# Optimization experiments

Measured on AMD Instinct MI355X. Metric: run time of the kernel, lower is better.

Reference implementation:

```python
import jax, jax.numpy as jnp
import numpy as np

B, T, D = 2, 2048, 1024
H = 16
HD = D // H  # 64


def _rope_tables(t_len, hd, dtype=jnp.float32):
    inv_freq = 1.0 / (10000.0 ** (jnp.arange(0, hd, 2, dtype=jnp.float32) / hd))
    freqs = jnp.outer(jnp.arange(t_len, dtype=jnp.float32), inv_freq)  # [T, hd/2]
    emb = jnp.concatenate([freqs, freqs], axis=-1)  # [T, hd]
    return emb.astype(dtype)


def _rotate_half(x):
    x1, x2 = jnp.split(x, 2, axis=-1)
    return jnp.concatenate([-x2, x1], axis=-1)


def setup_inputs() -> dict:
    key = jax.random.key(0)
    k1, k2, k3 = jax.random.split(key, 3)
    x = jax.random.normal(k1, (B, T, D), dtype=jnp.float32)
    w_qkv = jax.random.normal(k2, (D, 3 * D), dtype=jnp.float32) * (D ** -0.5)
    w_out = jax.random.normal(k3, (D, D), dtype=jnp.float32) * (D ** -0.5)
    return {"x": x, "w_qkv": w_qkv, "w_out": w_out}


def reference(x, w_qkv, w_out):
    Bc, Tc, Dc = x.shape
    scale = HD ** -0.5
    qkv = x @ w_qkv  # [B,T,3D]
    q, k, v = jnp.split(qkv, 3, axis=-1)
    # -> [B,H,T,hd]
    q = q.reshape(Bc, Tc, H, HD).transpose(0, 2, 1, 3)
    k = k.reshape(Bc, Tc, H, HD).transpose(0, 2, 1, 3)
    v = v.reshape(Bc, Tc, H, HD).transpose(0, 2, 1, 3)
    emb = _rope_tables(Tc, HD, x.dtype)  # [T,hd]
    cos = jnp.cos(emb)[None, None, :, :]
    sin = jnp.sin(emb)[None, None, :, :]
    q = q * cos + _rotate_half(q) * sin
    k = k * cos + _rotate_half(k) * sin
    attn = jnp.einsum('bhqd,bhkd->bhqk', q, k) * scale  # [B,H,T,T]
    causal = jnp.tril(jnp.ones((Tc, Tc), dtype=bool))
    attn = jnp.where(causal[None, None], attn, -jnp.inf)
    attn = jax.nn.softmax(attn, axis=-1)
    out = jnp.einsum('bhqk,bhkd->bhqd', attn, v)
    out = out.transpose(0, 2, 1, 3).reshape(Bc, Tc, Dc)
    return out @ w_out
```

## Files before the change

### kernel.cpp

```cpp
#include <hip/hip_runtime.h>

#define TSEQ 2048
#define DMODEL 1024
#define NHEAD 16
#define HDIM 64
#define NB 2
#define MROWS 4096
#define NQKV 3072
#define QSCALE 0.1803368801111204f
#define NEGINF -3.0e38f

using s16x8 = __attribute__((ext_vector_type(8))) short;
using s16x4 = __attribute__((ext_vector_type(4))) short;
using f32x4 = __attribute__((ext_vector_type(4))) float;
using u32x2 = __attribute__((ext_vector_type(2))) unsigned int;

static __device__ __forceinline__ float b2f(unsigned short u) {
  union { unsigned int i; float f; } x; x.i = ((unsigned int)u) << 16; return x.f;
}
static __device__ __forceinline__ unsigned short f2b(float f) {
  unsigned int u = __float_as_uint(f);
  u += 0x7fffu + ((u >> 16) & 1u);
  return (unsigned short)(u >> 16);
}

typedef const __attribute__((address_space(1))) char gchar;
typedef __attribute__((address_space(3))) char lchar;
static __device__ __forceinline__ void gload_lds16(const void* g, void* l) {
  __builtin_amdgcn_global_load_lds((gchar*)g, (lchar*)l, 16, 0, 0);
}

__global__ __launch_bounds__(256) void k_prep(const float* __restrict__ x,
                                              short* __restrict__ xb,
                                              const float* __restrict__ wq,
                                              short* __restrict__ wqT,
                                              const float* __restrict__ wo,
                                              short* __restrict__ woT) {
  __shared__ float tile[32][33];
  const int blk = blockIdx.x;
  const int tid = threadIdx.x;
  if (blk < 4096) {
    const int i = blk * 256 + tid;
    const float4 v = ((const float4*)x)[i];
    s16x4 o;
    o.x = (short)f2b(v.x); o.y = (short)f2b(v.y);
    o.z = (short)f2b(v.z); o.w = (short)f2b(v.w);
    ((s16x4*)xb)[i] = o;
    return;
  }
  const float* in; short* out; int C, bx, by;
  if (blk < 7168) {
    const int l = blk - 4096; in = wq; out = wqT; C = NQKV;
    bx = l % 96; by = l / 96;
  } else {
    const int l = blk - 7168; in = wo; out = woT; C = DMODEL;
    bx = l & 31; by = l >> 5;
  }
  const int tx = tid & 31, ty4 = (tid >> 5) * 4;
#pragma unroll
  for (int i = 0; i < 4; ++i)
    tile[ty4 + i][tx] = in[(by * 32 + ty4 + i) * C + bx * 32 + tx];
  __syncthreads();
#pragma unroll
  for (int i = 0; i < 4; ++i)
    out[(bx * 32 + ty4 + i) * DMODEL + by * 32 + tx] = (short)f2b(tile[tx][ty4 + i]);
}

template <int IM, bool OUT_BF16>
__global__ __launch_bounds__(256) void k_gemm(const short* __restrict__ A,
                                              const short* __restrict__ BT,
                                              void* __restrict__ Cv,
                                              int M, int N, int K) {
  __shared__ __attribute__((aligned(16))) short As[IM * 32 * 32];
  __shared__ __attribute__((aligned(16))) short Bs[128 * 32];
  const int tid = threadIdx.x;
  const int wave = tid >> 6, lane = tid & 63, quad = lane >> 4, l15 = lane & 15;
  const int wm = (wave >> 1) * (IM * 16), wn = (wave & 1) * 64;
  const int m0 = blockIdx.y * (IM * 32), n0 = blockIdx.x * 128;
  f32x4 acc[IM][4] = {};
  const int r0 = tid >> 2, g0 = (tid & 3) ^ ((r0 >> 1) & 3);
  const int r1 = (tid + 256) >> 2, g1 = (tid & 3) ^ ((r1 >> 1) & 3);
  const char* Ab = (const char*)A;
  const char* Bb = (const char*)BT;
  char* AsB = (char*)As;
  char* BsB = (char*)Bs;
  const int ldsw0 = wave * 1024;
  const int ldsw1 = 4096 + wave * 1024;
  const long a0off = ((long)(m0 + r0) * K) * 2 + g0 * 16;
  const long a1off = ((long)(m0 + r1) * K) * 2 + g1 * 16;
  const long b0off = ((long)(n0 + r0) * K) * 2 + g0 * 16;
  const long b1off = ((long)(n0 + r1) * K) * 2 + g1 * 16;
  for (int k0 = 0; k0 < K; k0 += 32) {
    __syncthreads();
    gload_lds16(Ab + a0off + k0 * 2, AsB + ldsw0);
    if (IM == 4) gload_lds16(Ab + a1off + k0 * 2, AsB + ldsw1);
    gload_lds16(Bb + b0off + k0 * 2, BsB + ldsw0);
    gload_lds16(Bb + b1off + k0 * 2, BsB + ldsw1);
    __syncthreads();
    s16x8 af[IM], bf[4];
#pragma unroll
    for (int i = 0; i < IM; ++i) {
      const int ra = wm + i * 16 + l15;
      af[i] = *(const s16x8*)(AsB + ra * 64 + ((quad ^ ((ra >> 1) & 3)) * 16));
    }
#pragma unroll
    for (int j = 0; j < 4; ++j) {
      const int rb = wn + j * 16 + l15;
      bf[j] = *(const s16x8*)(BsB + rb * 64 + ((quad ^ ((rb >> 1) & 3)) * 16));
    }
#pragma unroll
    for (int i = 0; i < IM; ++i)
#pragma unroll
      for (int j = 0; j < 4; ++j)
        acc[i][j] = __builtin_amdgcn_mfma_f32_16x16x32_bf16(af[i], bf[j], acc[i][j], 0, 0, 0);
  }
#pragma unroll
  for (int i = 0; i < IM; ++i) {
    const int row = m0 + wm + i * 16 + quad * 4;
#pragma unroll
    for (int j = 0; j < 4; ++j) {
      const int col = n0 + wn + j * 16 + l15;
#pragma unroll
      for (int r = 0; r < 4; ++r) {
        if (OUT_BF16) ((short*)Cv)[(long)(row + r) * N + col] = (short)f2b(acc[i][j][r]);
        else          ((float*)Cv)[(long)(row + r) * N + col] = acc[i][j][r];
      }
    }
  }
}

__global__ __launch_bounds__(256) void k_rope_rearrange(const short* __restrict__ qkv,
                                                        short* __restrict__ Q,
                                                        short* __restrict__ Ko,
                                                        short* __restrict__ Vt) {
  __shared__ float vt[64][65];
  const int tt = blockIdx.x;
  const int h = blockIdx.y;
  const int b = blockIdx.z;
  const int bh = b * NHEAD + h;
  const int tid = threadIdx.x;
#pragma unroll
  for (int it = 0; it < 16; ++it) {
    const int idx = it * 256 + tid;
    const int tl = idx >> 6;
    const int d = idx & 63;
    const int t = tt * 64 + tl;
    const int base = (b * TSEQ + t) * NQKV + h * HDIM + d;
    const float qv = b2f((unsigned short)qkv[base]);
    const float kv = b2f((unsigned short)qkv[base + DMODEL]);
    const float vv = b2f((unsigned short)qkv[base + 2 * DMODEL]);
    const int pd = (d < 32) ? 32 : -32;
    const float qp = b2f((unsigned short)qkv[base + pd]);
    const float kp = b2f((unsigned short)qkv[base + DMODEL + pd]);
    const int fi = d & 31;
    const float inv = exp2f(-(float)fi * (13.2877123795494f / 32.0f));
    const float ang = (float)t * inv;
    float sn, cs;
    __sincosf(ang, &sn, &cs);
    const float sgn = (d < 32) ? -1.0f : 1.0f;
    const float qo = (qv * cs + sgn * qp * sn) * QSCALE;
    const float ko = kv * cs + sgn * kp * sn;
    const int ob = (bh * TSEQ + t) * HDIM + d;
    Q[ob] = (short)f2b(qo);
    Ko[ob] = (short)f2b(ko);
    vt[tl][d] = vv;
  }
  __syncthreads();
#pragma unroll
  for (int it = 0; it < 16; ++it) {
    const int idx = it * 256 + tid;
    const int d = idx >> 6;
    const int tl = idx & 63;
    Vt[(bh * HDIM + d) * TSEQ + tt * 64 + tl] = (short)f2b(vt[tl][d]);
  }
}

__global__ __launch_bounds__(256) __attribute__((amdgpu_waves_per_eu(4)))
void k_attn(const short* __restrict__ Qg,
            const short* __restrict__ Kg,
            const short* __restrict__ Vg,
            short* __restrict__ O) {
  __shared__ __attribute__((aligned(16))) short Ks[2][64 * 64];
  __shared__ __attribute__((aligned(16))) short Vs[2][64 * 64];
  __shared__ __attribute__((aligned(16))) short pl[4][16 * 64];
  const int bx = blockIdx.x, by = blockIdx.y;
  const int r_ = (bx & 7) ^ (by & 7);
  const int idx_ = ((bx >> 3) + (by >> 3)) & 3;
  const int qi = (idx_ == 0) ? r_ : (idx_ == 1) ? 15 - r_ : (idx_ == 2) ? 16 + r_ : 31 - r_;
  const int bh = by;
  const int b = bh >> 4, h = bh & 15;
  const int tid = threadIdx.x, wave = tid >> 6, lane = tid & 63;
  const int quad = lane >> 4, l15 = lane & 15;
  const char* Kb = (const char*)(Kg + (long)bh * TSEQ * HDIM);
  const char* Vb = (const char*)(Vg + (long)bh * HDIM * TSEQ);
  const short* Qb = Qg + (long)bh * TSEQ * HDIM;
  const int qr0 = qi * 64 + wave * 16;
  const s16x8 aq0 = *(const s16x8*)&Qb[(qr0 + l15) * HDIM + quad * 8];
  const s16x8 aq1 = *(const s16x8*)&Qb[(qr0 + l15) * HDIM + 32 + quad * 8];
  f32x4 o[4] = {};
  float lsum = 0.0f;
  const int kr0 = tid >> 3, kg0 = (tid & 7) ^ (kr0 & 7);
  const int kr1 = (tid + 256) >> 3, kg1 = (tid & 7) ^ (kr1 & 7);
  char* KsB = (char*)Ks;
  char* VsB = (char*)Vs;
  char* plwB = (char*)pl + wave * 2048;
  const int ldsw0 = wave * 1024, ldsw1 = 4096 + wave * 1024;

#define STAGE(kjv, buf)                                                     \
  do {                                                                      \
    const char* Kt_ = Kb + (kjv) * 8192;                                    \
    const char* Vt_ = Vb + (kjv) * 128;                                     \
    char* kd_ = KsB + (buf) * 8192;                                         \
    char* vd_ = VsB + (buf) * 8192;                                         \
    gload_lds16(Kt_ + (kr0 * 8 + kg0) * 16, kd_ + ldsw0);                   \
    gload_lds16(Kt_ + (kr1 * 8 + kg1) * 16, kd_ + ldsw1);                   \
    gload_lds16(Vt_ + kr0 * (TSEQ * 2) + kg0 * 16, vd_ + ldsw0);            \
    gload_lds16(Vt_ + kr1 * (TSEQ * 2) + kg1 * 16, vd_ + ldsw1);            \
  } while (0)

  STAGE(0, 0);
  __syncthreads();

  for (int kj = 0; kj <= qi; ++kj) {
    const int cur = kj & 1;
    if (kj < qi) STAGE(kj + 1, cur ^ 1);
    const char* kb = KsB + cur * 8192;
    const char* vb = VsB + cur * 8192;

    f32x4 s[4];
#pragma unroll
    for (int j2 = 0; j2 < 4; ++j2) {
      const int row = j2 * 16 + l15;
      const s16x8 k0 = *(const s16x8*)(kb + row * 128 + ((quad ^ (row & 7)) * 16));
      const s16x8 k1 = *(const s16x8*)(kb + row * 128 + (((4 + quad) ^ (row & 7)) * 16));
      f32x4 z = {};
      z = __builtin_amdgcn_mfma_f32_16x16x32_bf16(k0, aq0, z, 0, 0, 0);
      z = __builtin_amdgcn_mfma_f32_16x16x32_bf16(k1, aq1, z, 0, 0, 0);
      s[j2] = z;
    }
    if (kj == qi) {
      const int q_loc = wave * 16 + l15;
#pragma unroll
      for (int j2 = 0; j2 < 4; ++j2)
#pragma unroll
        for (int r = 0; r < 4; ++r)
          if (j2 * 16 + quad * 4 + r > q_loc) s[j2][r] = NEGINF;
    }
    float ps = 0.0f;
#pragma unroll
    for (int j2 = 0; j2 < 4; ++j2) {
      const unsigned int u0 = __float_as_uint(exp2f(s[j2][0])) & 0xffff0000u;
      const unsigned int u1 = __float_as_uint(exp2f(s[j2][1])) & 0xffff0000u;
      const unsigned int u2 = __float_as_uint(exp2f(s[j2][2])) & 0xffff0000u;
      const unsigned int u3 = __float_as_uint(exp2f(s[j2][3])) & 0xffff0000u;
      ps += __uint_as_float(u0) + __uint_as_float(u1) +
            __uint_as_float(u2) + __uint_as_float(u3);
      u32x2 w;
      w.x = (u0 >> 16) | u1;
      w.y = (u2 >> 16) | u3;
      const int t0 = j2 * 16 + quad * 4;
      *(u32x2*)(plwB + l15 * 128 + (((t0 >> 3) ^ (l15 & 7)) * 16) + (quad & 1) * 8) = w;
    }
    lsum += ps;
    const s16x8 bp0 = *(const s16x8*)(plwB + l15 * 128 + ((quad ^ (l15 & 7)) * 16));
    const s16x8 bp1 = *(const s16x8*)(plwB + l15 * 128 + (((4 + quad) ^ (l15 & 7)) * 16));
#pragma unroll
    for (int hs = 0; hs < 4; ++hs) {
      const int d = hs * 16 + l15;
      const s16x8 av0 = *(const s16x8*)(vb + d * 128 + ((quad ^ (d & 7)) * 16));
      const s16x8 av1 = *(const s16x8*)(vb + d * 128 + (((4 + quad) ^ (d & 7)) * 16));
      o[hs] = __builtin_amdgcn_mfma_f32_16x16x32_bf16(av0, bp0, o[hs], 0, 0, 0);
      o[hs] = __builtin_amdgcn_mfma_f32_16x16x32_bf16(av1, bp1, o[hs], 0, 0, 0);
    }
    __syncthreads();
  }
#undef STAGE
  lsum += __shfl_xor(lsum, 16);
  lsum += __shfl_xor(lsum, 32);
  const float rinv = 1.0f / lsum;
  const int t = qi * 64 + wave * 16 + l15;
  short* Orow = O + (long)(b * TSEQ + t) * DMODEL + h * HDIM + quad * 4;
#pragma unroll
  for (int hs = 0; hs < 4; ++hs) {
    s16x4 w;
    w.x = (short)f2b(o[hs][0] * rinv);
    w.y = (short)f2b(o[hs][1] * rinv);
    w.z = (short)f2b(o[hs][2] * rinv);
    w.w = (short)f2b(o[hs][3] * rinv);
    *(s16x4*)(Orow + hs * 16) = w;
  }
}

extern "C" void kernel_launch(void* const* d_in, const int* in_sizes, int n_in,
                              void* d_out, int out_size, void* d_ws, size_t ws_size,
                              hipStream_t stream) {
  const float* x = (const float*)d_in[0];
  const float* w_qkv = (const float*)d_in[1];
  const float* w_out = (const float*)d_in[2];
  float* out = (float*)d_out;
  char* ws = (char*)d_ws;

  short* xb    = (short*)(ws);
  short* wqkvT = (short*)(ws + (8ll << 20));
  short* woutT = (short*)(ws + (14ll << 20));
  short* qkvb  = (short*)(ws + (16ll << 20));
  short* Ob    = qkvb;
  short* Qb    = (short*)(ws + (40ll << 20));
  short* Kb    = (short*)(ws + (48ll << 20));
  short* Vt    = (short*)(ws + (56ll << 20));

  k_prep<<<dim3(8192), dim3(256), 0, stream>>>(x, xb, w_qkv, wqkvT, w_out, woutT);
  k_gemm<4, true><<<dim3(NQKV / 128, MROWS / 128), dim3(256), 0, stream>>>(
      xb, wqkvT, (void*)qkvb, MROWS, NQKV, DMODEL);
  k_rope_rearrange<<<dim3(TSEQ / 64, NHEAD, NB), dim3(256), 0, stream>>>(qkvb, Qb, Kb, Vt);
  k_attn<<<dim3(TSEQ / 64, NB * NHEAD), dim3(256), 0, stream>>>(Qb, Kb, Vt, Ob);
  k_gemm<2, false><<<dim3(DMODEL / 128, MROWS / 64), dim3(256), 0, stream>>>(
      Ob, woutT, (void*)out, MROWS, DMODEL, DMODEL);
}
```

Before: 195.2 us.

## Fuse RoPE and Q/K/V head rearrangement into the QKV GEMM epilogue

Replaces the separate rope/rearrange kernel with a specialized QKV GEMM whose epilogue applies rotary embedding and scale to the Q and K tiles and writes V transposed directly. Each wave's 64-column tile maps onto exactly one head, so the rotate-half pairs (d, d+32) sit in the same thread's accumulators. This removes one kernel launch and a full bf16 round trip of the qkv intermediate through global memory. In exchange the epilogue does scattered 2-byte stores and extra sincos work per output element.

Measured after the change: 197.7 us. About the same (+1.3%).

```diff
diff --git a/kernel.cpp b/kernel.cpp
--- a/kernel.cpp
+++ b/kernel.cpp
@@ -8,6 +8,7 @@
 #define MROWS 4096
 #define NQKV 3072
 #define QSCALE 0.1803368801111204f
+#define ROPE_C (13.2877123795494f / 32.0f)
 #define NEGINF -3.0e38f
 
 using s16x8 = __attribute__((ext_vector_type(8))) short;
@@ -64,6 +65,97 @@
 #pragma unroll
   for (int i = 0; i < 4; ++i)
     out[(bx * 32 + ty4 + i) * DMODEL + by * 32 + tx] = (short)f2b(tile[tx][ty4 + i]);
+}
+
+__global__ __launch_bounds__(256) void k_gemm_qkv(const short* __restrict__ A,
+                                                  const short* __restrict__ BT,
+                                                  short* __restrict__ Qo,
+                                                  short* __restrict__ Ko,
+                                                  short* __restrict__ Vt) {
+  __shared__ __attribute__((aligned(16))) short As[128 * 32];
+  __shared__ __attribute__((aligned(16))) short Bs[128 * 32];
+  const int K = DMODEL, N = NQKV;
+  const int tid = threadIdx.x;
+  const int wave = tid >> 6, lane = tid & 63, quad = lane >> 4, l15 = lane & 15;
+  const int wm = (wave >> 1) * 64, wn = (wave & 1) * 64;
+  const int m0 = blockIdx.y * 128, n0 = blockIdx.x * 128;
+  f32x4 acc[4][4] = {};
+  const int r0 = tid >> 2, g0 = (tid & 3) ^ ((r0 >> 1) & 3);
+  const int r1 = (tid + 256) >> 2, g1 = (tid & 3) ^ ((r1 >> 1) & 3);
+  const char* Ab = (const char*)A;
+  const char* Bb = (const char*)BT;
+  char* AsB = (char*)As;
+  char* BsB = (char*)Bs;
+  const int ldsw0 = wave * 1024;
+  const int ldsw1 = 4096 + wave * 1024;
+  const long a0off = ((long)(m0 + r0) * K) * 2 + g0 * 16;
+  const long a1off = ((long)(m0 + r1) * K) * 2 + g1 * 16;
+  const long b0off = ((long)(n0 + r0) * K) * 2 + g0 * 16;
+  const long b1off = ((long)(n0 + r1) * K) * 2 + g1 * 16;
+  for (int k0 = 0; k0 < K; k0 += 32) {
+    __syncthreads();
+    gload_lds16(Ab + a0off + k0 * 2, AsB + ldsw0);
+    gload_lds16(Ab + a1off + k0 * 2, AsB + ldsw1);
+    gload_lds16(Bb + b0off + k0 * 2, BsB + ldsw0);
+    gload_lds16(Bb + b1off + k0 * 2, BsB + ldsw1);
+    __syncthreads();
+    s16x8 af[4], bf[4];
+#pragma unroll
+    for (int i = 0; i < 4; ++i) {
+      const int ra = wm + i * 16 + l15;
+      af[i] = *(const s16x8*)(AsB + ra * 64 + ((quad ^ ((ra >> 1) & 3)) * 16));
+      const int rb = wn + i * 16 + l15;
+      bf[i] = *(const s16x8*)(BsB + rb * 64 + ((quad ^ ((rb >> 1) & 3)) * 16));
+    }
+#pragma unroll
+    for (int i = 0; i < 4; ++i)
+#pragma unroll
+      for (int j = 0; j < 4; ++j)
+        acc[i][j] = __builtin_amdgcn_mfma_f32_16x16x32_bf16(af[i], bf[j], acc[i][j], 0, 0, 0);
+  }
+  const int colbase = n0 + wn;
+  const int region = colbase >> 10;
+  const int hh = (colbase & 1023) >> 6;
+  const int bq = m0 >> 11;
+  const int tbase = (m0 & 2047) + wm;
+  if (region == 2) {
+    short* dst = Vt + (((long)(bq * NHEAD + hh) * HDIM) << 11);
+#pragma unroll
+    for (int i = 0; i < 4; ++i) {
+      const int t0 = tbase + i * 16 + quad * 4;
+#pragma unroll
+      for (int j = 0; j < 4; ++j) {
+        const int d = j * 16 + l15;
+        s16x4 w;
+        w.x = (short)f2b(acc[i][j][0]);
+        w.y = (short)f2b(acc[i][j][1]);
+        w.z = (short)f2b(acc[i][j][2]);
+        w.w = (short)f2b(acc[i][j][3]);
+        *(s16x4*)(dst + (((long)d) << 11) + t0) = w;
+      }
+    }
+  } else {
+    short* dst = (region ? Ko : Qo) + (long)(bq * NHEAD + hh) * TSEQ * HDIM;
+    const float qs = region ? 1.0f : QSCALE;
+    const float inv0 = exp2f(-(float)l15 * ROPE_C);
+    const float inv1 = exp2f(-(float)(16 + l15) * ROPE_C);
+#pragma unroll
+    for (int i = 0; i < 4; ++i) {
+#pragma unroll
+      for (int r = 0; r < 4; ++r) {
+        const int t = tbase + i * 16 + quad * 4 + r;
+        float sn0, cs0, sn1, cs1;
+        __sincosf((float)t * inv0, &sn0, &cs0);
+        __sincosf((float)t * inv1, &sn1, &cs1);
+        sn0 *= qs; cs0 *= qs; sn1 *= qs; cs1 *= qs;
+        short* drow = dst + (long)t * HDIM;
+        drow[l15]      = (short)f2b(acc[i][0][r] * cs0 - acc[i][2][r] * sn0);
+        drow[16 + l15] = (short)f2b(acc[i][1][r] * cs1 - acc[i][3][r] * sn1);
+        drow[32 + l15] = (short)f2b(acc[i][2][r] * cs0 + acc[i][0][r] * sn0);
+        drow[48 + l15] = (short)f2b(acc[i][3][r] * cs1 + acc[i][1][r] * sn1);
+      }
+    }
+  }
 }
 
 template <int IM, bool OUT_BF16>
@@ -126,52 +218,6 @@
         else          ((float*)Cv)[(long)(row + r) * N + col] = acc[i][j][r];
       }
     }
-  }
-}
-
-__global__ __launch_bounds__(256) void k_rope_rearrange(const short* __restrict__ qkv,
-                                                        short* __restrict__ Q,
-                                                        short* __restrict__ Ko,
-                                                        short* __restrict__ Vt) {
-  __shared__ float vt[64][65];
-  const int tt = blockIdx.x;
-  const int h = blockIdx.y;
-  const int b = blockIdx.z;
-  const int bh = b * NHEAD + h;
-  const int tid = threadIdx.x;
-#pragma unroll
-  for (int it = 0; it < 16; ++it) {
-    const int idx = it * 256 + tid;
-    const int tl = idx >> 6;
-    const int d = idx & 63;
-    const int t = tt * 64 + tl;
-    const int base = (b * TSEQ + t) * NQKV + h * HDIM + d;
-    const float qv = b2f((unsigned short)qkv[base]);
-    const float kv = b2f((unsigned short)qkv[base + DMODEL]);
-    const float vv = b2f((unsigned short)qkv[base + 2 * DMODEL]);
-    const int pd = (d < 32) ? 32 : -32;
-    const float qp = b2f((unsigned short)qkv[base + pd]);
-    const float kp = b2f((unsigned short)qkv[base + DMODEL + pd]);
-    const int fi = d & 31;
-    const float inv = exp2f(-(float)fi * (13.2877123795494f / 32.0f));
-    const float ang = (float)t * inv;
-    float sn, cs;
-    __sincosf(ang, &sn, &cs);
-    const float sgn = (d < 32) ? -1.0f : 1.0f;
-    const float qo = (qv * cs + sgn * qp * sn) * QSCALE;
-    const float ko = kv * cs + sgn * kp * sn;
-    const int ob = (bh * TSEQ + t) * HDIM + d;
-    Q[ob] = (short)f2b(qo);
-    Ko[ob] = (short)f2b(ko);
-    vt[tl][d] = vv;
-  }
-  __syncthreads();
-#pragma unroll
-  for (int it = 0; it < 16; ++it) {
-    const int idx = it * 256 + tid;
-    const int d = idx >> 6;
-    const int tl = idx & 63;
-    Vt[(bh * HDIM + d) * TSEQ + tt * 64 + tl] = (short)f2b(vt[tl][d]);
   }
 }
 
@@ -303,16 +349,14 @@
   short* xb    = (short*)(ws);
   short* wqkvT = (short*)(ws + (8ll << 20));
   short* woutT = (short*)(ws + (14ll << 20));
-  short* qkvb  = (short*)(ws + (16ll << 20));
-  short* Ob    = qkvb;
-  short* Qb    = (short*)(ws + (40ll << 20));
-  short* Kb    = (short*)(ws + (48ll << 20));
-  short* Vt    = (short*)(ws + (56ll << 20));
+  short* Qb    = (short*)(ws + (16ll << 20));
+  short* Kb    = (short*)(ws + (24ll << 20));
+  short* Vt    = (short*)(ws + (32ll << 20));
+  short* Ob    = (short*)(ws + (40ll << 20));
 
   k_prep<<<dim3(8192), dim3(256), 0, stream>>>(x, xb, w_qkv, wqkvT, w_out, woutT);
-  k_gemm<4, true><<<dim3(NQKV / 128, MROWS / 128), dim3(256), 0, stream>>>(
-      xb, wqkvT, (void*)qkvb, MROWS, NQKV, DMODEL);
-  k_rope_rearrange<<<dim3(TSEQ / 64, NHEAD, NB), dim3(256), 0, stream>>>(qkvb, Qb, Kb, Vt);
+  k_gemm_qkv<<<dim3(NQKV / 128, MROWS / 128), dim3(256), 0, stream>>>(
+      xb, wqkvT, Qb, Kb, Vt);
   k_attn<<<dim3(TSEQ / 64, NB * NHEAD), dim3(256), 0, stream>>>(Qb, Kb, Vt, Ob);
   k_gemm<2, false><<<dim3(DMODEL / 128, MROWS / 64), dim3(256), 0, stream>>>(
       Ob, woutT, (void*)out, MROWS, DMODEL, DMODEL);
```
